# Kernel optimization log

Measured on AMD Instinct MI355X. Metric: run time of the kernel, lower is better.

## Reference

```python
import jax, jax.numpy as jnp
import numpy as np

N_GROUPS = 40
MAX_DISPARITY = 48


def _groupwise(l, r, n_groups):
    # l, r: (N, C, H, W') -> (N, G, H, W') mean over channels within each group
    n, c, h, w = l.shape
    return (l * r).reshape(n, n_groups, c // n_groups, h, w).mean(axis=2)


def setup_inputs() -> dict:
    key = jax.random.key(0)
    k1, k2 = jax.random.split(key)
    left = jax.random.normal(k1, (4, 320, 80, 160), dtype=jnp.float32)
    right = jax.random.normal(k2, (4, 320, 80, 160), dtype=jnp.float32)
    return {"left": left, "right": right}


def reference(left, right):
    # Output: (N, n_groups, H, W, max_disparity) cost volume.
    n, c, h, w = left.shape
    slices = []
    for d in range(MAX_DISPARITY):  # static, small, structurally distinct shifts
        if d == 0:
            cost = _groupwise(left, right, N_GROUPS)
        else:
            cost = _groupwise(left[:, :, :, d:], right[:, :, :, : w - d], N_GROUPS)
            cost = jnp.pad(cost, ((0, 0), (0, 0), (0, 0), (d, 0)))  # zeros where w < d
        slices.append(cost)
    return jnp.stack(slices, axis=-1)
```

## Files before the change

kernel.cpp:

```cpp
#include <hip/hip_runtime.h>

typedef float f4 __attribute__((ext_vector_type(4)));

constexpr int N_  = 4;
constexpr int C_  = 320;
constexpr int H_  = 80;
constexpr int W_  = 160;
constexpr int G_  = 40;
constexpr int CPG = 8;
constexpr int D_  = 48;
constexpr int PAD = 48;
constexpr int RW  = PAD + W_;
constexpr int HW  = H_ * W_;
constexpr int TILES = (W_ / 4) * (D_ / 4);

__global__ __launch_bounds__(256) void gw_cost_kernel(const float* __restrict__ Lg,
                                                      const float* __restrict__ Rg,
                                                      float* __restrict__ out) {
    __shared__ float Ls[CPG * W_];
    __shared__ float Rs[CPG * RW];

    const int tid = threadIdx.x;
    const int blk = blockIdx.x;

    const int h = blk % H_;
    const int g = (blk / H_) % G_;
    const int n = blk / (H_ * G_);

    const size_t rowbase = (size_t)(n * C_ + g * CPG) * HW + (size_t)h * W_;

    if (tid < CPG * (PAD / 4)) {
        const int c = tid / 12, p4 = tid % 12;
        *(f4*)&Rs[c * RW + p4 * 4] = (f4)(0.0f);
    }

    const int wid  = tid >> 6;
    const int lane = tid & 63;
    if (lane < 40) {
        #pragma unroll
        for (int k = 0; k < 2; ++k) {
            const int c = wid + k * 4;
            const float* gl = Lg + rowbase + (size_t)c * HW + lane * 4;
            const float* gr = Rg + rowbase + (size_t)c * HW + lane * 4;
            __builtin_amdgcn_global_load_lds(
                (const __attribute__((address_space(1))) void*)gl,
                (__attribute__((address_space(3))) void*)&Ls[c * W_], 16, 0, 0);
            __builtin_amdgcn_global_load_lds(
                (const __attribute__((address_space(1))) void*)gr,
                (__attribute__((address_space(3))) void*)&Rs[c * RW + PAD], 16, 0, 0);
        }
    }
    __syncthreads();

    for (int t = tid; t < TILES; t += 256) {
        const int tw = t / 12;
        const int td = t % 12;
        const int w0 = tw * 4;
        const int d0 = td * 4;
        const int r0 = w0 - d0 + PAD;

        f4 acc0 = (f4)(0.0f), acc1 = (f4)(0.0f), acc2 = (f4)(0.0f), acc3 = (f4)(0.0f);

        #pragma unroll
        for (int c = 0; c < CPG; ++c) {
            const f4 lv = *(const f4*)&Ls[c * W_ + w0];
            const float* rp = &Rs[c * RW + (r0 - 4)];
            const f4 ra = *(const f4*)(rp);
            const f4 rb = *(const f4*)(rp + 4);
            float rr[8];
            #pragma unroll
            for (int k = 0; k < 4; ++k) { rr[k] = ra[k]; rr[4 + k] = rb[k]; }
            #pragma unroll
            for (int j = 0; j < 4; ++j) {
                acc0[j] += lv[0] * rr[4 + 0 - j];
                acc1[j] += lv[1] * rr[4 + 1 - j];
                acc2[j] += lv[2] * rr[4 + 2 - j];
                acc3[j] += lv[3] * rr[4 + 3 - j];
            }
        }

        float* op = out + (size_t)blk * (W_ * D_) + (size_t)w0 * D_ + d0;
        *(f4*)(op + 0 * D_) = acc0 * 0.125f;
        *(f4*)(op + 1 * D_) = acc1 * 0.125f;
        *(f4*)(op + 2 * D_) = acc2 * 0.125f;
        *(f4*)(op + 3 * D_) = acc3 * 0.125f;
    }
}

extern "C" void kernel_launch(void* const* d_in, const int* in_sizes, int n_in,
                              void* d_out, int out_size, void* d_ws, size_t ws_size,
                              hipStream_t stream) {
    const float* Lg = (const float*)d_in[0];
    const float* Rg = (const float*)d_in[1];
    float* out = (float*)d_out;

    const int nblocks = N_ * G_ * H_;
    gw_cost_kernel<<<dim3(nblocks), dim3(256), 0, stream>>>(Lg, Rg, out);
}
```

Before: 106.7 us.

## Give each wavefront an independent 40-column quarter-row task without block barriers

Each block now holds four independent wave tasks. Every wave loads its own quarter-row of left data plus a haloed right window into private LDS, zeros only the padding it needs, and waits on its own loads with vmcnt instead of __syncthreads. This removes block-wide synchronisation so waves can overlap loads and compute independently. The cost is redundant halo loads of right data across neighbouring quarters, and the block count grows from N*G*H to N*G*H*4/4, which is the same number of blocks.

```diff
diff --git a/kernel.cpp b/kernel.cpp
--- a/kernel.cpp
+++ b/kernel.cpp
@@ -9,62 +9,74 @@
 constexpr int G_  = 40;
 constexpr int CPG = 8;
 constexpr int D_  = 48;
-constexpr int PAD = 48;
-constexpr int RW  = PAD + W_;
 constexpr int HW  = H_ * W_;
-constexpr int TILES = (W_ / 4) * (D_ / 4);
+constexpr int QW  = 40;
+constexpr int NQ  = W_ / QW;
+constexpr int PADW = 48;
+constexpr int RWN  = PADW + QW;
+constexpr int TPW  = (QW / 4) * (D_ / 4);
 
 __global__ __launch_bounds__(256) void gw_cost_kernel(const float* __restrict__ Lg,
                                                       const float* __restrict__ Rg,
                                                       float* __restrict__ out) {
-    __shared__ float Ls[CPG * W_];
-    __shared__ float Rs[CPG * RW];
+    __shared__ float Ls[4][CPG][QW];
+    __shared__ float Rs[4][CPG][RWN];
 
-    const int tid = threadIdx.x;
-    const int blk = blockIdx.x;
+    const int tid  = threadIdx.x;
+    const int wid  = tid >> 6;
+    const int lane = tid & 63;
 
-    const int h = blk % H_;
-    const int g = (blk / H_) % G_;
-    const int n = blk / (H_ * G_);
+    const int task = blockIdx.x * 4 + wid;
+    const int q    = task & (NQ - 1);
+    const int row  = task >> 2;
+    const int h = row % H_;
+    const int g = (row / H_) % G_;
+    const int n = row / (H_ * G_);
+    const int w0q = q * QW;
 
-    const size_t rowbase = (size_t)(n * C_ + g * CPG) * HW + (size_t)h * W_;
+    const size_t base = (size_t)(n * C_ + g * CPG) * HW + (size_t)h * W_;
 
-    if (tid < CPG * (PAD / 4)) {
-        const int c = tid / 12, p4 = tid % 12;
-        *(f4*)&Rs[c * RW + p4 * 4] = (f4)(0.0f);
+    const int zl = (q == 0) ? PADW : (q == 1 ? 8 : 0);
+
+    if (lane * 4 < zl) {
+        #pragma unroll
+        for (int c = 0; c < CPG; ++c)
+            *(f4*)&Rs[wid][c][lane * 4] = (f4)(0.0f);
     }
 
-    const int wid  = tid >> 6;
-    const int lane = tid & 63;
-    if (lane < 40) {
-        #pragma unroll
-        for (int k = 0; k < 2; ++k) {
-            const int c = wid + k * 4;
-            const float* gl = Lg + rowbase + (size_t)c * HW + lane * 4;
-            const float* gr = Rg + rowbase + (size_t)c * HW + lane * 4;
+    const int goffR = w0q - PADW + zl;
+    const int nlR   = (RWN - zl) / 4;
+    #pragma unroll
+    for (int c = 0; c < CPG; ++c) {
+        if (lane < QW / 4) {
+            const float* gl = Lg + base + (size_t)c * HW + w0q + lane * 4;
             __builtin_amdgcn_global_load_lds(
                 (const __attribute__((address_space(1))) void*)gl,
-                (__attribute__((address_space(3))) void*)&Ls[c * W_], 16, 0, 0);
+                (__attribute__((address_space(3))) void*)&Ls[wid][c][0], 16, 0, 0);
+        }
+        if (lane < nlR) {
+            const float* gr = Rg + base + (size_t)c * HW + goffR + lane * 4;
             __builtin_amdgcn_global_load_lds(
                 (const __attribute__((address_space(1))) void*)gr,
-                (__attribute__((address_space(3))) void*)&Rs[c * RW + PAD], 16, 0, 0);
+                (__attribute__((address_space(3))) void*)&Rs[wid][c][zl], 16, 0, 0);
         }
     }
-    __syncthreads();
+    asm volatile("s_waitcnt vmcnt(0)" ::: "memory");
+    __builtin_amdgcn_sched_barrier(0);
 
-    for (int t = tid; t < TILES; t += 256) {
-        const int tw = t / 12;
-        const int td = t % 12;
-        const int w0 = tw * 4;
-        const int d0 = td * 4;
-        const int r0 = w0 - d0 + PAD;
+    for (int t = lane; t < TPW; t += 64) {
+        const int twl = t / 12;
+        const int td  = t % 12;
+        const int w0l = twl * 4;
+        const int d0  = td * 4;
+        const int r0  = w0l - d0 + PADW;
 
-        f4 acc0 = (f4)(0.0f), acc1 = (f4)(0.0f), acc2 = (f4)(0.0f), acc3 = (f4)(0.0f);
+        f4 a0 = (f4)(0.0f), a1 = (f4)(0.0f), a2 = (f4)(0.0f), a3 = (f4)(0.0f);
 
         #pragma unroll
         for (int c = 0; c < CPG; ++c) {
-            const f4 lv = *(const f4*)&Ls[c * W_ + w0];
-            const float* rp = &Rs[c * RW + (r0 - 4)];
+            const f4 lv = *(const f4*)&Ls[wid][c][w0l];
+            const float* rp = &Rs[wid][c][r0 - 4];
             const f4 ra = *(const f4*)(rp);
             const f4 rb = *(const f4*)(rp + 4);
             float rr[8];
@@ -72,18 +84,18 @@
             for (int k = 0; k < 4; ++k) { rr[k] = ra[k]; rr[4 + k] = rb[k]; }
             #pragma unroll
             for (int j = 0; j < 4; ++j) {
-                acc0[j] += lv[0] * rr[4 + 0 - j];
-                acc1[j] += lv[1] * rr[4 + 1 - j];
-                acc2[j] += lv[2] * rr[4 + 2 - j];
-                acc3[j] += lv[3] * rr[4 + 3 - j];
+                a0[j] += lv[0] * rr[4 + 0 - j];
+                a1[j] += lv[1] * rr[4 + 1 - j];
+                a2[j] += lv[2] * rr[4 + 2 - j];
+                a3[j] += lv[3] * rr[4 + 3 - j];
             }
         }
 
-        float* op = out + (size_t)blk * (W_ * D_) + (size_t)w0 * D_ + d0;
-        *(f4*)(op + 0 * D_) = acc0 * 0.125f;
-        *(f4*)(op + 1 * D_) = acc1 * 0.125f;
-        *(f4*)(op + 2 * D_) = acc2 * 0.125f;
-        *(f4*)(op + 3 * D_) = acc3 * 0.125f;
+        float* op = out + (size_t)row * (W_ * D_) + (size_t)(w0q + w0l) * D_ + d0;
+        *(f4*)(op + 0 * D_) = a0 * 0.125f;
+        *(f4*)(op + 1 * D_) = a1 * 0.125f;
+        *(f4*)(op + 2 * D_) = a2 * 0.125f;
+        *(f4*)(op + 3 * D_) = a3 * 0.125f;
     }
 }
 
@@ -94,6 +106,6 @@
     const float* Rg = (const float*)d_in[1];
     float* out = (float*)d_out;
 
-    const int nblocks = N_ * G_ * H_;
+    const int nblocks = (N_ * G_ * H_ * NQ) / 4;
     gw_cost_kernel<<<dim3(nblocks), dim3(256), 0, stream>>>(Lg, Rg, out);
 }
```

Result: slower. 117.3 us (+9.9%).
